# Performance work log

Measured on AMD Instinct MI355X. Metric: run time of the kernel, lower is better.

The kernel has to match this reference:

```python
import jax, jax.numpy as jnp
import numpy as np

B, S, E = 2, 2048, 1024
H, KVH, D = 16, 4, 64
ROPE_BASE = 10000.0


def setup_inputs() -> dict:
    key = jax.random.key(0)
    ks = jax.random.split(key, 7)
    s = 0.02
    return {
        "query_inputs": jax.random.normal(ks[0], (B, S, E), jnp.float32),
        "key_inputs": jax.random.normal(ks[1], (B, S, E), jnp.float32),
        "value_inputs": jax.random.normal(ks[2], (B, S, E), jnp.float32),
        "attention_mask": jnp.ones((1, 1, S, S), dtype=bool),
        "Wq": jax.random.normal(ks[3], (E, H * D), jnp.float32) * s,
        "Wk": jax.random.normal(ks[4], (E, KVH * D), jnp.float32) * s,
        "Wv": jax.random.normal(ks[5], (E, KVH * D), jnp.float32) * s,
        "Wo": jax.random.normal(ks[6], (H * D, E), jnp.float32) * s,
    }


def _rotate_half(x):
    x1, x2 = jnp.split(x, 2, axis=-1)
    return jnp.concatenate((-x2, x1), axis=-1)


def _rope(k, q):
    # standard RoPE, rescaling_factor=None -> base 10000
    d = q.shape[-1]
    inv_freq = 1.0 / (ROPE_BASE ** (jnp.arange(0, d, 2, dtype=jnp.float32) / d))
    t = jnp.arange(q.shape[1], dtype=jnp.float32)
    freqs = jnp.einsum("i,j->ij", t, inv_freq)          # [S, d/2]
    emb = jnp.concatenate((freqs, freqs), axis=-1)       # [S, d]
    cos = jnp.cos(emb)[None, :, None, :]                 # [1, S, 1, d]
    sin = jnp.sin(emb)[None, :, None, :]
    apply = lambda x: x * cos + _rotate_half(x) * sin
    return apply(k), apply(q)


def reference(query_inputs, key_inputs, value_inputs, attention_mask, Wq, Wk, Wv, Wo):
    q = (query_inputs @ Wq).reshape(B, S, H, D)
    k = (key_inputs @ Wk).reshape(B, S, KVH, D)
    v = (value_inputs @ Wv).reshape(B, S, KVH, D)
    k, q = _rope(k, q)
    n_rep = H // KVH
    k = jnp.repeat(k, n_rep, axis=2)                     # [B, S, H, D]
    v = jnp.repeat(v, n_rep, axis=2)
    logits = jnp.einsum("bthd,bThd->bhtT", q, k) / jnp.sqrt(jnp.float32(D))
    logits = jnp.where(attention_mask, logits, jnp.float32(-1e30))
    w = jax.nn.softmax(logits, axis=-1)                  # [B, H, S, S]
    out = jnp.einsum("bhtT,bThd->bthd", w, v).reshape(B, S, H * D)
    return out @ Wo
```

## Files before the change

### kernel.cpp

```cpp
#include <hip/hip_runtime.h>
#include <hip/hip_bf16.h>
#include <math.h>

#define Bsz 2
#define Sseq 2048
#define Edim 1024
#define Hq 16
#define KVH 4
#define Dh 64

typedef __attribute__((ext_vector_type(4))) float f32x4;
typedef __attribute__((ext_vector_type(16))) float f32x16;
typedef __attribute__((ext_vector_type(8))) short bf16x8;

__device__ inline unsigned short f2bf(float f) {
    union { float f; unsigned int u; } v; v.f = f;
    unsigned int u = v.u;
    u += 0x7FFFu + ((u >> 16) & 1u);
    return (unsigned short)(u >> 16);
}

__device__ inline float bf2f(unsigned short u) {
    union { unsigned int u; float f; } v; v.u = (unsigned int)u << 16;
    return v.f;
}

__device__ inline unsigned int cvt_pk_bf16(float a, float b) {
    unsigned int r;
    asm("v_cvt_pk_bf16_f32 %0, %1, %2" : "=v"(r) : "v"(a), "v"(b));
    return r;
}

__device__ inline f32x4 mfma16(bf16x8 a, bf16x8 b, f32x4 c) {
    return __builtin_amdgcn_mfma_f32_16x16x32_bf16(a, b, c, 0, 0, 0);
}

__device__ inline f32x16 mfma32(bf16x8 a, bf16x8 b, f32x16 c) {
    return __builtin_amdgcn_mfma_f32_32x32x16_bf16(a, b, c, 0, 0, 0);
}

__device__ inline void gload_lds16(const void* g, void* l) {
    __builtin_amdgcn_global_load_lds(
        (const __attribute__((address_space(1))) unsigned int*)g,
        (__attribute__((address_space(3))) unsigned int*)l, 16, 0, 0);
}

__global__ __launch_bounds__(256)
void prep(const float* __restrict__ Xq, const float* __restrict__ Xk,
          const float* __restrict__ Xv,
          const float* __restrict__ Wq, const float* __restrict__ Wk,
          const float* __restrict__ Wv, const float* __restrict__ Wo,
          unsigned short* __restrict__ Xq_b, unsigned short* __restrict__ Xk_b,
          unsigned short* __restrict__ Xv_b,
          unsigned short* __restrict__ Wq_t, unsigned short* __restrict__ Wk_t,
          unsigned short* __restrict__ Wv_t, unsigned short* __restrict__ Wo_t,
          float* __restrict__ tab) {
    int bid = blockIdx.x;
    if (bid < 256) {
        int idx = bid * 256 + threadIdx.x;
        int s = idx >> 5, j = idx & 31;
        double inv = pow(10000.0, -(double)(2 * j) / 64.0);
        double a = (double)s * inv;
        tab[idx * 2 + 0] = (float)cos(a);
        tab[idx * 2 + 1] = (float)sin(a);
        return;
    }
    bid -= 256;
    if (bid < 12288) {
        const float* X; unsigned short* Y;
        if (bid < 4096)      { X = Xq; Y = Xq_b; }
        else if (bid < 8192) { X = Xk; Y = Xk_b; bid -= 4096; }
        else                 { X = Xv; Y = Xv_b; bid -= 8192; }
        int i = bid * 256 + threadIdx.x;
        float4 v = ((const float4*)X)[i];
        ushort4 o;
        o.x = f2bf(v.x); o.y = f2bf(v.y); o.z = f2bf(v.z); o.w = f2bf(v.w);
        ((ushort4*)Y)[i] = o;
        return;
    }
    bid -= 12288;
    const float* W; unsigned short* Wt; int N; int local;
    if (bid < 1024)      { W = Wq; Wt = Wq_t; N = 1024; local = bid; }
    else if (bid < 1280) { W = Wk; Wt = Wk_t; N = 256;  local = bid - 1024; }
    else if (bid < 1536) { W = Wv; Wt = Wv_t; N = 256;  local = bid - 1280; }
    else                 { W = Wo; Wt = Wo_t; N = 1024; local = bid - 1536; }
    __shared__ float tile[32][33];
    int nb = N >> 5;
    int bn = (local % nb) * 32, bk = (local / nb) * 32;
    int tx = threadIdx.x & 31, ty = threadIdx.x >> 5;
    #pragma unroll
    for (int i = 0; i < 32; i += 8)
        tile[ty + i][tx] = W[(size_t)(bk + ty + i) * N + bn + tx];
    __syncthreads();
    #pragma unroll
    for (int i = 0; i < 32; i += 8)
        Wt[(size_t)(bn + ty + i) * 1024 + bk + tx] = f2bf(tile[tx][ty + i]);
}

__global__ __launch_bounds__(256)
void qkv_gemm(const unsigned short* __restrict__ Xq_b,
              const unsigned short* __restrict__ Xk_b,
              const unsigned short* __restrict__ Xv_b,
              const unsigned short* __restrict__ Wq_t,
              const unsigned short* __restrict__ Wk_t,
              const unsigned short* __restrict__ Wv_t,
              unsigned short* __restrict__ Qb,
              unsigned short* __restrict__ Kbf,
              unsigned short* __restrict__ Vt,
              const float* __restrict__ tab, float qscale) {
    __shared__ __attribute__((aligned(16))) unsigned short Alds[128 * 64];
    __shared__ __attribute__((aligned(16))) unsigned short Blds[128 * 64];

    int bid = blockIdx.x;
    const unsigned short *A, *Bt;
    unsigned short* C;
    int m0, n0, N, epi;
    float prescale;
    if (bid < 256) {
        A = Xq_b; Bt = Wq_t; C = Qb;
        m0 = (bid & 31) << 7; n0 = (bid >> 5) << 7; N = 1024; epi = 0; prescale = qscale;
    } else if (bid < 320) {
        int l = bid - 256;
        A = Xk_b; Bt = Wk_t; C = Kbf;
        m0 = (l & 31) << 7; n0 = (l >> 5) << 7; N = 256; epi = 0; prescale = 1.f;
    } else {
        int l = bid - 320;
        A = Xv_b; Bt = Wv_t; C = Vt;
        m0 = (l & 31) << 7; n0 = (l >> 5) << 7; N = 256; epi = 1; prescale = 1.f;
    }

    const int t = threadIdx.x;
    const int wid = t >> 6, lane = t & 63;
    const int l15 = lane & 15, l4 = lane >> 4;
    const int wm = (wid >> 1) * 64, wn = (wid & 1) * 64;

    f32x4 acc[4][4] = {};

    for (int k0 = 0; k0 < 1024; k0 += 64) {
        #pragma unroll
        for (int i = 0; i < 4; ++i) {
            int slot = t + 256 * i;
            int row = slot >> 3, ch = slot & 7;
            int g = ch ^ (row & 7);
            gload_lds16(A + (size_t)(m0 + row) * 1024 + k0 + g * 8, &Alds[slot * 8]);
            gload_lds16(Bt + (size_t)(n0 + row) * 1024 + k0 + g * 8, &Blds[slot * 8]);
        }
        __syncthreads();
        __builtin_amdgcn_s_setprio(1);
        #pragma unroll
        for (int kc = 0; kc < 2; ++kc) {
            bf16x8 af[4], bfr[4];
            #pragma unroll
            for (int mt = 0; mt < 4; ++mt)
                af[mt] = *(const bf16x8*)&Alds[(wm + mt * 16 + l15) * 64 + (((kc * 4 + l4) ^ (l15 & 7)) * 8)];
            #pragma unroll
            for (int nt = 0; nt < 4; ++nt)
                bfr[nt] = *(const bf16x8*)&Blds[(wn + nt * 16 + l15) * 64 + (((kc * 4 + l4) ^ (l15 & 7)) * 8)];
            #pragma unroll
            for (int mt = 0; mt < 4; ++mt)
                #pragma unroll
                for (int nt = 0; nt < 4; ++nt)
                    acc[mt][nt] = mfma16(af[mt], bfr[nt], acc[mt][nt]);
        }
        __builtin_amdgcn_s_setprio(0);
        __syncthreads();
    }

    if (epi == 0) {
        #pragma unroll
        for (int mt = 0; mt < 4; ++mt) {
            int rbase = m0 + wm + mt * 16 + 4 * l4;
            #pragma unroll
            for (int nt = 0; nt < 2; ++nt) {
                int col = n0 + wn + nt * 16 + l15;
                int j = col & 31;
                #pragma unroll
                for (int r = 0; r < 4; ++r) {
                    int row = rbase + r;
                    int s = row & (Sseq - 1);
                    float c = tab[(s * 32 + j) * 2 + 0];
                    float sn = tab[(s * 32 + j) * 2 + 1];
                    float x1 = acc[mt][nt][r] * prescale;
                    float x2 = acc[mt][nt + 2][r] * prescale;
                    C[(size_t)row * N + col]      = f2bf(x1 * c - x2 * sn);
                    C[(size_t)row * N + col + 32] = f2bf(x2 * c + x1 * sn);
                }
            }
        }
    } else {
        #pragma unroll
        for (int mt = 0; mt < 4; ++mt)
            #pragma unroll
            for (int nt = 0; nt < 4; ++nt)
                #pragma unroll
                for (int r = 0; r < 4; ++r) {
                    int row = m0 + wm + mt * 16 + 4 * l4 + r;
                    int col = n0 + wn + nt * 16 + l15;
                    int b = row >> 11, s = row & (Sseq - 1);
                    C[((size_t)(b * 256 + col) << 11) + s] = f2bf(acc[mt][nt][r]);
                }
    }
}

__global__ __launch_bounds__(256)
void wo_gemm(const unsigned short* __restrict__ A,
             const unsigned short* __restrict__ Bt,
             float* __restrict__ C) {
    __shared__ __attribute__((aligned(16))) unsigned short Alds[128 * 64];
    __shared__ __attribute__((aligned(16))) unsigned short Blds[128 * 64];
    const int t = threadIdx.x;
    const int wid = t >> 6, lane = t & 63;
    const int l15 = lane & 15, l4 = lane >> 4;
    const int m0 = blockIdx.x * 128, n0 = blockIdx.y * 128;
    const int wm = (wid >> 1) * 64, wn = (wid & 1) * 64;

    f32x4 acc[4][4] = {};

    for (int k0 = 0; k0 < 1024; k0 += 64) {
        #pragma unroll
        for (int i = 0; i < 4; ++i) {
            int slot = t + 256 * i;
            int row = slot >> 3, ch = slot & 7;
            int g = ch ^ (row & 7);
            gload_lds16(A + (size_t)(m0 + row) * 1024 + k0 + g * 8, &Alds[slot * 8]);
            gload_lds16(Bt + (size_t)(n0 + row) * 1024 + k0 + g * 8, &Blds[slot * 8]);
        }
        __syncthreads();
        __builtin_amdgcn_s_setprio(1);
        #pragma unroll
        for (int kc = 0; kc < 2; ++kc) {
            bf16x8 af[4], bfr[4];
            #pragma unroll
            for (int mt = 0; mt < 4; ++mt)
                af[mt] = *(const bf16x8*)&Alds[(wm + mt * 16 + l15) * 64 + (((kc * 4 + l4) ^ (l15 & 7)) * 8)];
            #pragma unroll
            for (int nt = 0; nt < 4; ++nt)
                bfr[nt] = *(const bf16x8*)&Blds[(wn + nt * 16 + l15) * 64 + (((kc * 4 + l4) ^ (l15 & 7)) * 8)];
            #pragma unroll
            for (int mt = 0; mt < 4; ++mt)
                #pragma unroll
                for (int nt = 0; nt < 4; ++nt)
                    acc[mt][nt] = mfma16(af[mt], bfr[nt], acc[mt][nt]);
        }
        __builtin_amdgcn_s_setprio(0);
        __syncthreads();
    }

    #pragma unroll
    for (int mt = 0; mt < 4; ++mt)
        #pragma unroll
        for (int nt = 0; nt < 4; ++nt)
            #pragma unroll
            for (int r = 0; r < 4; ++r)
                C[(size_t)(m0 + wm + mt * 16 + 4 * l4 + r) * 1024 + n0 + wn + nt * 16 + l15]
                    = acc[mt][nt][r];
}

__global__ __launch_bounds__(256, 4)
void attn_split(const unsigned short* __restrict__ Q,
                const unsigned short* __restrict__ Kb,
                const unsigned short* __restrict__ Vt,
                unsigned short* __restrict__ Op,
                float* __restrict__ Lp) {
    __shared__ __attribute__((aligned(16))) unsigned short Klds[2][64 * 64];
    __shared__ __attribute__((aligned(16))) unsigned short Vlds[2][64 * 64];

    const int t = threadIdx.x, wid = t >> 6, lane = t & 63;
    const int l31 = lane & 31, hi = lane >> 5;
    const int q0 = blockIdx.x * 128;
    const int bh = blockIdx.y;
    const int half = blockIdx.z;
    const int b = bh >> 4, h = bh & 15, kvh = h >> 2;
    const int qb0 = (b << 11) + q0 + wid * 32;
    const int kh0 = half * 1024;

    bf16x8 qf[4];
    {
        const unsigned short* qp = Q + (size_t)(qb0 + l31) * 1024 + h * 64 + hi * 8;
        #pragma unroll
        for (int kc = 0; kc < 4; ++kc)
            qf[kc] = *(const bf16x8*)(qp + kc * 16);
    }

    f32x16 accO[2] = {};
    float lrow = 0.f;

    #define STAGE(buf, kt)                                                              \
        do {                                                                            \
            int kbase = kh0 + (kt) * 64;                                                \
            _Pragma("unroll")                                                           \
            for (int i = 0; i < 2; ++i) {                                               \
                int slot = t + 256 * i;                                                 \
                int row = slot >> 3, ch = slot & 7;                                     \
                int g = ch ^ (row & 7);                                                 \
                gload_lds16(Kb + ((size_t)((b << 11) + kbase + row) << 8) + kvh * 64 + g * 8, \
                            &Klds[buf][slot * 8]);                                      \
                gload_lds16(Vt + ((size_t)((b * 4 + kvh) * 64 + row) << 11) + kbase + g * 8,  \
                            &Vlds[buf][slot * 8]);                                      \
            }                                                                           \
        } while (0)

    STAGE(0, 0);
    asm volatile("s_waitcnt vmcnt(0)");
    __syncthreads();

    int cur = 0;
    for (int kt = 0; kt < 16; ++kt) {
        if (kt + 1 < 16) STAGE(cur ^ 1, kt + 1);

        f32x16 sacc[2] = {};
        __builtin_amdgcn_s_setprio(1);
        #pragma unroll
        for (int kc = 0; kc < 4; ++kc) {
            #pragma unroll
            for (int kb = 0; kb < 2; ++kb) {
                int row = kb * 32 + l31;
                bf16x8 kf = *(const bf16x8*)
                    &Klds[cur][row * 64 + (((kc * 2 + hi) ^ (row & 7)) * 8)];
                sacc[kb] = mfma32(kf, qf[kc], sacc[kb]);
            }
        }
        __builtin_amdgcn_s_setprio(0);

        float pv[2][16];
        float rs = 0.f;
        #pragma unroll
        for (int kb = 0; kb < 2; ++kb)
            #pragma unroll
            for (int r = 0; r < 16; ++r) {
                float p = __builtin_amdgcn_exp2f(sacc[kb][r]);
                pv[kb][r] = p;
                rs += p;
            }
        lrow += rs + __shfl_xor(rs, 32);

        bf16x8 pa[4];
        #pragma unroll
        for (int kb = 0; kb < 2; ++kb) {
            #pragma unroll
            for (int hf = 0; hf < 2; ++hf) {
                const float* p = &pv[kb][hf * 8];
                unsigned int u0 = cvt_pk_bf16(p[0], p[1]);
                unsigned int u1 = cvt_pk_bf16(p[2], p[3]);
                unsigned int u2 = cvt_pk_bf16(p[4], p[5]);
                unsigned int u3 = cvt_pk_bf16(p[6], p[7]);
                asm("v_permlane32_swap_b32 %0, %1" : "+v"(u0), "+v"(u2));
                asm("v_permlane32_swap_b32 %0, %1" : "+v"(u1), "+v"(u3));
                uint4 w; w.x = u0; w.y = u1; w.z = u2; w.w = u3;
                pa[kb * 2 + hf] = *(bf16x8*)&w;
            }
        }

        __builtin_amdgcn_s_setprio(1);
        #pragma unroll
        for (int kq = 0; kq < 4; ++kq) {
            #pragma unroll
            for (int db = 0; db < 2; ++db) {
                int row = db * 32 + l31;
                bf16x8 vf = *(const bf16x8*)
                    &Vlds[cur][row * 64 + (((kq * 2 + hi) ^ (row & 7)) * 8)];
                accO[db] = mfma32(pa[kq], vf, accO[db]);
            }
        }
        __builtin_amdgcn_s_setprio(0);

        asm volatile("s_waitcnt vmcnt(0)");
        __syncthreads();
        cur ^= 1;
    }
    #undef STAGE

    float linv = __builtin_amdgcn_rcpf(lrow);
    unsigned short* Oh = Op + (size_t)half * 4194304;
    #pragma unroll
    for (int r = 0; r < 16; ++r) {
        int q = (r & 3) + 8 * (r >> 2) + 4 * hi;
        float li = __shfl(linv, q);
        #pragma unroll
        for (int db = 0; db < 2; ++db)
            Oh[(size_t)(qb0 + q) * 1024 + h * 64 + db * 32 + l31] = f2bf(accO[db][r] * li);
    }
    if (hi == 0)
        Lp[half * 65536 + (bh << 11) + q0 + wid * 32 + l31] = lrow;
}

__global__ __launch_bounds__(256)
void combine(const unsigned short* __restrict__ Op, const float* __restrict__ Lp,
             unsigned short* __restrict__ AttO) {
    const int q = blockIdx.x, t = threadIdx.x;
    const int b = q >> 11, s = q & 2047, h = t >> 4;
    const int bh = (b << 4) | h;
    float l0 = Lp[(bh << 11) + s];
    float l1 = Lp[65536 + (bh << 11) + s];
    float w = __builtin_amdgcn_rcpf(l0 + l1);
    float w0 = l0 * w, w1 = l1 * w;
    size_t idx = (size_t)q * 1024 + t * 4;
    ushort4 a = *(const ushort4*)(Op + idx);
    ushort4 c = *(const ushort4*)(Op + 4194304 + idx);
    ushort4 o;
    o.x = f2bf(w0 * bf2f(a.x) + w1 * bf2f(c.x));
    o.y = f2bf(w0 * bf2f(a.y) + w1 * bf2f(c.y));
    o.z = f2bf(w0 * bf2f(a.z) + w1 * bf2f(c.z));
    o.w = f2bf(w0 * bf2f(a.w) + w1 * bf2f(c.w));
    *(ushort4*)(AttO + idx) = o;
}

extern "C" void kernel_launch(void* const* d_in, const int* in_sizes, int n_in,
                              void* d_out, int out_size, void* d_ws, size_t ws_size,
                              hipStream_t stream) {
    const float* Xq = (const float*)d_in[0];
    const float* Xk = (const float*)d_in[1];
    const float* Xv = (const float*)d_in[2];
    const float* Wq = (const float*)d_in[4];
    const float* Wk = (const float*)d_in[5];
    const float* Wv = (const float*)d_in[6];
    const float* Wo = (const float*)d_in[7];

    char* ws = (char*)d_ws;
    unsigned short* Xq_b = (unsigned short*)(ws + 0);
    unsigned short* Xk_b = (unsigned short*)(ws + 8388608);
    unsigned short* Xv_b = (unsigned short*)(ws + 16777216);
    unsigned short* Qb   = (unsigned short*)(ws + 25165824);
    unsigned short* Kbf  = (unsigned short*)(ws + 33554432);
    unsigned short* Vt   = (unsigned short*)(ws + 35651584);
    unsigned short* AttO = (unsigned short*)(ws + 37748736);
    unsigned short* Wq_t = (unsigned short*)(ws + 46137344);
    unsigned short* Wk_t = (unsigned short*)(ws + 48234496);
    unsigned short* Wv_t = (unsigned short*)(ws + 48758784);
    unsigned short* Wo_t = (unsigned short*)(ws + 49283072);
    float*          tab  = (float*)(ws + 51380224);
    unsigned short* Op   = (unsigned short*)(ws + 0);
    float*          Lp   = (float*)(ws + 16777216);

    prep<<<dim3(15104), 256, 0, stream>>>(Xq, Xk, Xv, Wq, Wk, Wv, Wo,
                                          Xq_b, Xk_b, Xv_b,
                                          Wq_t, Wk_t, Wv_t, Wo_t, tab);

    const float qscale = 0.125f * 1.44269504088896340736f;
    qkv_gemm<<<dim3(384), 256, 0, stream>>>(Xq_b, Xk_b, Xv_b, Wq_t, Wk_t, Wv_t,
                                            Qb, Kbf, Vt, tab, qscale);

    attn_split<<<dim3(16, 32, 2), 256, 0, stream>>>(Qb, Kbf, Vt, Op, Lp);
    combine<<<dim3(4096), 256, 0, stream>>>(Op, Lp, AttO);

    wo_gemm<<<dim3(32, 8), 256, 0, stream>>>(AttO, Wo_t, (float*)d_out);
}
```

Measured before the change: 112.4 us.

## Halve GEMM N-tile to 64 for more blocks; precompute attention load pointers

Shrinks the QKV and Wo GEMM tiles from 128x128 to 128x64, with each wave owning 32 rows by 64 columns. This doubles the grid to 768 and 512 blocks, giving better occupancy of the CUs on MI355X. The attention kernel now precomputes its K/V global load pointers once and advances them each stage, replacing per-stage address arithmetic. It also splits the row-sum accumulation into two-wide vector partial sums. The cost is less operand reuse per block, so more global and LDS traffic per unit of MFMA work.

```diff
diff --git a/kernel.cpp b/kernel.cpp
--- a/kernel.cpp
+++ b/kernel.cpp
@@ -9,6 +9,7 @@
 #define KVH 4
 #define Dh 64
 
+typedef __attribute__((ext_vector_type(2))) float f32x2;
 typedef __attribute__((ext_vector_type(4))) float f32x4;
 typedef __attribute__((ext_vector_type(16))) float f32x16;
 typedef __attribute__((ext_vector_type(8))) short bf16x8;
@@ -109,32 +110,32 @@
               unsigned short* __restrict__ Vt,
               const float* __restrict__ tab, float qscale) {
     __shared__ __attribute__((aligned(16))) unsigned short Alds[128 * 64];
-    __shared__ __attribute__((aligned(16))) unsigned short Blds[128 * 64];
+    __shared__ __attribute__((aligned(16))) unsigned short Blds[64 * 64];
 
     int bid = blockIdx.x;
     const unsigned short *A, *Bt;
     unsigned short* C;
     int m0, n0, N, epi;
     float prescale;
-    if (bid < 256) {
+    if (bid < 512) {
         A = Xq_b; Bt = Wq_t; C = Qb;
-        m0 = (bid & 31) << 7; n0 = (bid >> 5) << 7; N = 1024; epi = 0; prescale = qscale;
-    } else if (bid < 320) {
-        int l = bid - 256;
+        m0 = (bid & 31) << 7; n0 = (bid >> 5) << 6; N = 1024; epi = 0; prescale = qscale;
+    } else if (bid < 640) {
+        int l = bid - 512;
         A = Xk_b; Bt = Wk_t; C = Kbf;
-        m0 = (l & 31) << 7; n0 = (l >> 5) << 7; N = 256; epi = 0; prescale = 1.f;
+        m0 = (l & 31) << 7; n0 = (l >> 5) << 6; N = 256; epi = 0; prescale = 1.f;
     } else {
-        int l = bid - 320;
+        int l = bid - 640;
         A = Xv_b; Bt = Wv_t; C = Vt;
-        m0 = (l & 31) << 7; n0 = (l >> 5) << 7; N = 256; epi = 1; prescale = 1.f;
+        m0 = (l & 31) << 7; n0 = (l >> 5) << 6; N = 256; epi = 1; prescale = 1.f;
     }
 
     const int t = threadIdx.x;
     const int wid = t >> 6, lane = t & 63;
     const int l15 = lane & 15, l4 = lane >> 4;
-    const int wm = (wid >> 1) * 64, wn = (wid & 1) * 64;
-
-    f32x4 acc[4][4] = {};
+    const int wm = wid * 32;
+
+    f32x4 acc[2][4] = {};
 
     for (int k0 = 0; k0 < 1024; k0 += 64) {
         #pragma unroll
@@ -143,21 +144,27 @@
             int row = slot >> 3, ch = slot & 7;
             int g = ch ^ (row & 7);
             gload_lds16(A + (size_t)(m0 + row) * 1024 + k0 + g * 8, &Alds[slot * 8]);
+        }
+        #pragma unroll
+        for (int i = 0; i < 2; ++i) {
+            int slot = t + 256 * i;
+            int row = slot >> 3, ch = slot & 7;
+            int g = ch ^ (row & 7);
             gload_lds16(Bt + (size_t)(n0 + row) * 1024 + k0 + g * 8, &Blds[slot * 8]);
         }
         __syncthreads();
         __builtin_amdgcn_s_setprio(1);
         #pragma unroll
         for (int kc = 0; kc < 2; ++kc) {
-            bf16x8 af[4], bfr[4];
-            #pragma unroll
-            for (int mt = 0; mt < 4; ++mt)
+            bf16x8 af[2], bfr[4];
+            #pragma unroll
+            for (int mt = 0; mt < 2; ++mt)
                 af[mt] = *(const bf16x8*)&Alds[(wm + mt * 16 + l15) * 64 + (((kc * 4 + l4) ^ (l15 & 7)) * 8)];
             #pragma unroll
             for (int nt = 0; nt < 4; ++nt)
-                bfr[nt] = *(const bf16x8*)&Blds[(wn + nt * 16 + l15) * 64 + (((kc * 4 + l4) ^ (l15 & 7)) * 8)];
-            #pragma unroll
-            for (int mt = 0; mt < 4; ++mt)
+                bfr[nt] = *(const bf16x8*)&Blds[(nt * 16 + l15) * 64 + (((kc * 4 + l4) ^ (l15 & 7)) * 8)];
+            #pragma unroll
+            for (int mt = 0; mt < 2; ++mt)
                 #pragma unroll
                 for (int nt = 0; nt < 4; ++nt)
                     acc[mt][nt] = mfma16(af[mt], bfr[nt], acc[mt][nt]);
@@ -168,11 +175,11 @@
 
     if (epi == 0) {
         #pragma unroll
-        for (int mt = 0; mt < 4; ++mt) {
+        for (int mt = 0; mt < 2; ++mt) {
             int rbase = m0 + wm + mt * 16 + 4 * l4;
             #pragma unroll
             for (int nt = 0; nt < 2; ++nt) {
-                int col = n0 + wn + nt * 16 + l15;
+                int col = n0 + nt * 16 + l15;
                 int j = col & 31;
                 #pragma unroll
                 for (int r = 0; r < 4; ++r) {
@@ -189,13 +196,13 @@
         }
     } else {
         #pragma unroll
-        for (int mt = 0; mt < 4; ++mt)
+        for (int mt = 0; mt < 2; ++mt)
             #pragma unroll
             for (int nt = 0; nt < 4; ++nt)
                 #pragma unroll
                 for (int r = 0; r < 4; ++r) {
                     int row = m0 + wm + mt * 16 + 4 * l4 + r;
-                    int col = n0 + wn + nt * 16 + l15;
+                    int col = n0 + nt * 16 + l15;
                     int b = row >> 11, s = row & (Sseq - 1);
                     C[((size_t)(b * 256 + col) << 11) + s] = f2bf(acc[mt][nt][r]);
                 }
@@ -207,14 +214,14 @@
              const unsigned short* __restrict__ Bt,
              float* __restrict__ C) {
     __shared__ __attribute__((aligned(16))) unsigned short Alds[128 * 64];
-    __shared__ __attribute__((aligned(16))) unsigned short Blds[128 * 64];
+    __shared__ __attribute__((aligned(16))) unsigned short Blds[64 * 64];
     const int t = threadIdx.x;
     const int wid = t >> 6, lane = t & 63;
     const int l15 = lane & 15, l4 = lane >> 4;
-    const int m0 = blockIdx.x * 128, n0 = blockIdx.y * 128;
-    const int wm = (wid >> 1) * 64, wn = (wid & 1) * 64;
-
-    f32x4 acc[4][4] = {};
+    const int m0 = blockIdx.x * 128, n0 = blockIdx.y * 64;
+    const int wm = wid * 32;
+
+    f32x4 acc[2][4] = {};
 
     for (int k0 = 0; k0 < 1024; k0 += 64) {
         #pragma unroll
@@ -223,21 +230,27 @@
             int row = slot >> 3, ch = slot & 7;
             int g = ch ^ (row & 7);
             gload_lds16(A + (size_t)(m0 + row) * 1024 + k0 + g * 8, &Alds[slot * 8]);
+        }
+        #pragma unroll
+        for (int i = 0; i < 2; ++i) {
+            int slot = t + 256 * i;
+            int row = slot >> 3, ch = slot & 7;
+            int g = ch ^ (row & 7);
             gload_lds16(Bt + (size_t)(n0 + row) * 1024 + k0 + g * 8, &Blds[slot * 8]);
         }
         __syncthreads();
         __builtin_amdgcn_s_setprio(1);
         #pragma unroll
         for (int kc = 0; kc < 2; ++kc) {
-            bf16x8 af[4], bfr[4];
-            #pragma unroll
-            for (int mt = 0; mt < 4; ++mt)
+            bf16x8 af[2], bfr[4];
+            #pragma unroll
+            for (int mt = 0; mt < 2; ++mt)
                 af[mt] = *(const bf16x8*)&Alds[(wm + mt * 16 + l15) * 64 + (((kc * 4 + l4) ^ (l15 & 7)) * 8)];
             #pragma unroll
             for (int nt = 0; nt < 4; ++nt)
-                bfr[nt] = *(const bf16x8*)&Blds[(wn + nt * 16 + l15) * 64 + (((kc * 4 + l4) ^ (l15 & 7)) * 8)];
-            #pragma unroll
-            for (int mt = 0; mt < 4; ++mt)
+                bfr[nt] = *(const bf16x8*)&Blds[(nt * 16 + l15) * 64 + (((kc * 4 + l4) ^ (l15 & 7)) * 8)];
+            #pragma unroll
+            for (int mt = 0; mt < 2; ++mt)
                 #pragma unroll
                 for (int nt = 0; nt < 4; ++nt)
                     acc[mt][nt] = mfma16(af[mt], bfr[nt], acc[mt][nt]);
@@ -247,12 +260,12 @@
     }
 
     #pragma unroll
-    for (int mt = 0; mt < 4; ++mt)
+    for (int mt = 0; mt < 2; ++mt)
         #pragma unroll
         for (int nt = 0; nt < 4; ++nt)
             #pragma unroll
             for (int r = 0; r < 4; ++r)
-                C[(size_t)(m0 + wm + mt * 16 + 4 * l4 + r) * 1024 + n0 + wn + nt * 16 + l15]
+                C[(size_t)(m0 + wm + mt * 16 + 4 * l4 + r) * 1024 + n0 + nt * 16 + l15]
                     = acc[mt][nt][r];
 }
 
@@ -282,31 +295,34 @@
             qf[kc] = *(const bf16x8*)(qp + kc * 16);
     }
 
+    const int r0 = t >> 3, c0 = t & 7;
+    const int g0 = c0 ^ (r0 & 7);
+    const int r1 = r0 + 32;
+    const int g1 = c0 ^ (r1 & 7);
+    const unsigned short* kp0 = Kb + (((size_t)((b << 11) + kh0 + r0)) << 8) + kvh * 64 + g0 * 8;
+    const unsigned short* kp1 = Kb + (((size_t)((b << 11) + kh0 + r1)) << 8) + kvh * 64 + g1 * 8;
+    const unsigned short* vp0 = Vt + (((size_t)((b * 4 + kvh) * 64 + r0)) << 11) + kh0 + g0 * 8;
+    const unsigned short* vp1 = Vt + (((size_t)((b * 4 + kvh) * 64 + r1)) << 11) + kh0 + g1 * 8;
+
     f32x16 accO[2] = {};
     float lrow = 0.f;
 
-    #define STAGE(buf, kt)                                                              \
-        do {                                                                            \
-            int kbase = kh0 + (kt) * 64;                                                \
-            _Pragma("unroll")                                                           \
-            for (int i = 0; i < 2; ++i) {                                               \
-                int slot = t + 256 * i;                                                 \
-                int row = slot >> 3, ch = slot & 7;                                     \
-                int g = ch ^ (row & 7);                                                 \
-                gload_lds16(Kb + ((size_t)((b << 11) + kbase + row) << 8) + kvh * 64 + g * 8, \
-                            &Klds[buf][slot * 8]);                                      \
-                gload_lds16(Vt + ((size_t)((b * 4 + kvh) * 64 + row) << 11) + kbase + g * 8,  \
-                            &Vlds[buf][slot * 8]);                                      \
-            }                                                                           \
+    #define STAGE(buf)                                                    \
+        do {                                                              \
+            gload_lds16(kp0, &Klds[buf][t * 8]);                          \
+            gload_lds16(kp1, &Klds[buf][(t + 256) * 8]);                  \
+            gload_lds16(vp0, &Vlds[buf][t * 8]);                          \
+            gload_lds16(vp1, &Vlds[buf][(t + 256) * 8]);                  \
+            kp0 += 64 * 256; kp1 += 64 * 256; vp0 += 64; vp1 += 64;       \
         } while (0)
 
-    STAGE(0, 0);
+    STAGE(0);
     asm volatile("s_waitcnt vmcnt(0)");
     __syncthreads();
 
     int cur = 0;
     for (int kt = 0; kt < 16; ++kt) {
-        if (kt + 1 < 16) STAGE(cur ^ 1, kt + 1);
+        if (kt + 1 < 16) STAGE(cur ^ 1);
 
         f32x16 sacc[2] = {};
         __builtin_amdgcn_s_setprio(1);
@@ -323,15 +339,18 @@
         __builtin_amdgcn_s_setprio(0);
 
         float pv[2][16];
-        float rs = 0.f;
+        f32x2 rs2 = {0.f, 0.f};
         #pragma unroll
         for (int kb = 0; kb < 2; ++kb)
             #pragma unroll
-            for (int r = 0; r < 16; ++r) {
-                float p = __builtin_amdgcn_exp2f(sacc[kb][r]);
-                pv[kb][r] = p;
-                rs += p;
+            for (int r = 0; r < 16; r += 2) {
+                float p0 = __builtin_amdgcn_exp2f(sacc[kb][r]);
+                float p1 = __builtin_amdgcn_exp2f(sacc[kb][r + 1]);
+                pv[kb][r] = p0;
+                pv[kb][r + 1] = p1;
+                rs2 += (f32x2){p0, p1};
             }
+        float rs = rs2[0] + rs2[1];
         lrow += rs + __shfl_xor(rs, 32);
 
         bf16x8 pa[4];
@@ -437,11 +456,11 @@
                                           Wq_t, Wk_t, Wv_t, Wo_t, tab);
 
     const float qscale = 0.125f * 1.44269504088896340736f;
-    qkv_gemm<<<dim3(384), 256, 0, stream>>>(Xq_b, Xk_b, Xv_b, Wq_t, Wk_t, Wv_t,
+    qkv_gemm<<<dim3(768), 256, 0, stream>>>(Xq_b, Xk_b, Xv_b, Wq_t, Wk_t, Wv_t,
                                             Qb, Kbf, Vt, tab, qscale);
 
     attn_split<<<dim3(16, 32, 2), 256, 0, stream>>>(Qb, Kbf, Vt, Op, Lp);
     combine<<<dim3(4096), 256, 0, stream>>>(Op, Lp, AttO);
 
-    wo_gemm<<<dim3(32, 8), 256, 0, stream>>>(AttO, Wo_t, (float*)d_out);
-}
+    wo_gemm<<<dim3(32, 16), 256, 0, stream>>>(AttO, Wo_t, (float*)d_out);
+}
```

Result: faster. 104.3 us (-7.2%).
